# Performance work log

Hardware: AMD Instinct MI355X
Metric: run time of the kernel (lower is better)

## Reference

```python
import jax, jax.numpy as jnp
import numpy as np

NUM_WIRES = 4
NUM_LAYERS = 2


def _apply_ry(state, w, theta):
    # state: (N, 2,2,2,2); theta: scalar or (N,)
    st = jnp.moveaxis(state, 1 + w, -1)
    c = jnp.cos(theta / 2)
    s = jnp.sin(theta / 2)
    # broadcast (N,) -> (N,1,1,1) against st[...,k] of shape (N,2,2,2)
    c = c.reshape(c.shape + (1,) * (st.ndim - 1 - c.ndim))
    s = s.reshape(s.shape + (1,) * (st.ndim - 1 - s.ndim))
    a0, a1 = st[..., 0], st[..., 1]
    st = jnp.stack([c * a0 - s * a1, s * a0 + c * a1], axis=-1)
    return jnp.moveaxis(st, -1, 1 + w)


def _apply_rz(state, w, theta):
    st = jnp.moveaxis(state, 1 + w, -1)
    p = jnp.exp(-0.5j * theta)  # phase on |0>; conj on |1>
    st = jnp.stack([st[..., 0] * p, st[..., 1] * jnp.conj(p)], axis=-1)
    return jnp.moveaxis(st, -1, 1 + w)


def _apply_cnot(state, cw, tw):
    st = jnp.moveaxis(state, (1 + cw, 1 + tw), (-2, -1))
    st = jnp.stack([st[..., 0, :], st[..., 1, ::-1]], axis=-2)
    return jnp.moveaxis(st, (-2, -1), (1 + cw, 1 + tw))


def _circuit(angles, params):
    # angles: (N, 4) RY input angles; params: (L, 4, 3)
    N = angles.shape[0]
    state = jnp.zeros((N, 2, 2, 2, 2), jnp.complex64).at[:, 0, 0, 0, 0].set(1.0)
    for i in range(NUM_WIRES):
        state = _apply_ry(state, i, angles[:, i])
    for l in range(NUM_LAYERS):
        for i in range(NUM_WIRES):
            state = _apply_ry(state, i, params[l, i, 0])
        for i in range(NUM_WIRES - 1):
            state = _apply_cnot(state, i, i + 1)
        for i in range(NUM_WIRES):
            state = _apply_ry(state, i, params[l, i, 1])
        for i in range(NUM_WIRES - 1):
            state = _apply_cnot(state, i + 1, i)
        for i in range(NUM_WIRES):
            state = _apply_rz(state, i, params[l, i, 2])
    probs = state.real ** 2 + state.imag ** 2  # (N,2,2,2,2)
    zs = []
    for i in range(NUM_WIRES):
        axes = tuple(a for a in range(1, 1 + NUM_WIRES) if a != 1 + i)
        marg = probs.sum(axis=axes)  # (N,2)
        zs.append(marg[:, 0] - marg[:, 1])
    return jnp.stack(zs, axis=1)  # (N,4)


def setup_inputs() -> dict:
    key = jax.random.key(0)
    kx, kp = jax.random.split(key)
    x = jax.random.normal(kx, (512, 28, 28), dtype=jnp.float32)
    params = jax.random.normal(kp, (NUM_LAYERS, NUM_WIRES, 3), dtype=jnp.float32)
    return {"x": x, "params": params}


def reference(x, params):
    B = x.shape[0]
    # extract non-overlapping 2x2 patches, row-major over (r, c), patch order
    # [x[r,c], x[r,c+1], x[r+1,c], x[r+1,c+1]] matching .view(batch, -1)
    patches = x.reshape(B, 14, 2, 14, 2).transpose(0, 1, 3, 2, 4).reshape(B, 196, 4)
    # per-patch-location scalar normalization over all batch*4 elements (ddof=1 std)
    n = B * 4
    m = patches.mean(axis=(0, 2), keepdims=True)
    sd = jnp.sqrt(((patches - m) ** 2).sum(axis=(0, 2), keepdims=True) / (n - 1))
    angles = (patches - m) / (sd + 1e-8) * jnp.pi
    z = _circuit(angles.reshape(B * 196, 4), params)  # (B*196, 4)
    return z.reshape(B, 196 * 4).astype(jnp.float32)
```

## Files before the change

kernel.cpp:

```cpp
#include <hip/hip_runtime.h>
#include <math.h>

#define BATCH   512
#define NPATCH  196
#define NSAMP   (BATCH * NPATCH)

__global__ __launch_bounds__(256) void stats_kernel(const float* __restrict__ x,
                                                    float2* __restrict__ stats) {
    const int p = blockIdx.x;
    const int r = p / 14, c = p - r * 14;
    const int t = threadIdx.x;

    float sum = 0.f, sq = 0.f;
    for (int b = t; b < BATCH; b += 256) {
        const float* base = x + b * 784 + (2 * r) * 28 + 2 * c;
        float2 v01 = *(const float2*)base;
        float2 v23 = *(const float2*)(base + 28);
        sum += v01.x + v01.y + v23.x + v23.y;
        sq  += v01.x * v01.x + v01.y * v01.y + v23.x * v23.x + v23.y * v23.y;
    }

    #pragma unroll
    for (int off = 32; off; off >>= 1) {
        sum += __shfl_down(sum, off, 64);
        sq  += __shfl_down(sq,  off, 64);
    }
    __shared__ float ssum[4], ssq[4];
    const int wave = t >> 6, lane = t & 63;
    if (lane == 0) { ssum[wave] = sum; ssq[wave] = sq; }
    __syncthreads();
    if (t == 0) {
        float S = ssum[0] + ssum[1] + ssum[2] + ssum[3];
        float Q = ssq[0]  + ssq[1]  + ssq[2]  + ssq[3];
        const float n = (float)(BATCH * 4);
        float m   = S / n;
        float var = (Q - S * S / n) / (n - 1.0f);
        float sd  = sqrtf(fmaxf(var, 0.f));
        float invh = 0.5f * 3.14159265358979323846f / (sd + 1e-8f);
        stats[p] = make_float2(m, invh);
    }
}

template <int MASK>
__device__ __forceinline__ void ry_gate(float* sr, float* si, float c, float s) {
    #pragma unroll
    for (int i = 0; i < 16; ++i) {
        if ((i & MASK) == 0) {
            const int j = i | MASK;
            float a0 = sr[i], a1 = sr[j];
            sr[i] = c * a0 - s * a1;
            sr[j] = s * a0 + c * a1;
            float b0 = si[i], b1 = si[j];
            si[i] = c * b0 - s * b1;
            si[j] = s * b0 + c * b1;
        }
    }
}

template <int CMASK, int TMASK>
__device__ __forceinline__ void cnot_gate(float* sr, float* si) {
    #pragma unroll
    for (int i = 0; i < 16; ++i) {
        if ((i & CMASK) && !(i & TMASK)) {
            const int j = i | TMASK;
            float t;
            t = sr[i]; sr[i] = sr[j]; sr[j] = t;
            t = si[i]; si[i] = si[j]; si[j] = t;
        }
    }
}

template <int MASK>
__device__ __forceinline__ void rz_gate(float* sr, float* si, float pc, float ps) {
    #pragma unroll
    for (int i = 0; i < 16; ++i) {
        float r = sr[i], im = si[i];
        if (i & MASK) { sr[i] = r * pc - im * ps; si[i] = im * pc + r * ps; }
        else          { sr[i] = r * pc + im * ps; si[i] = im * pc - r * ps; }
    }
}

__global__ __launch_bounds__(256) void circuit_kernel(const float* __restrict__ x,
                                                      const float* __restrict__ params,
                                                      const float2* __restrict__ stats,
                                                      float* __restrict__ out) {
    const int tid = blockIdx.x * 256 + threadIdx.x;
    if (tid >= NSAMP) return;
    const int b = tid / NPATCH;
    const int p = tid - b * NPATCH;
    const int r = p / 14, c = p - r * 14;

    const float* base = x + b * 784 + (2 * r) * 28 + 2 * c;
    float2 v01 = *(const float2*)base;
    float2 v23 = *(const float2*)(base + 28);
    float2 st  = stats[p];

    float h0 = (v01.x - st.x) * st.y;
    float h1 = (v01.y - st.x) * st.y;
    float h2 = (v23.x - st.x) * st.y;
    float h3 = (v23.y - st.x) * st.y;
    float c0, s0, c1, s1, c2, s2, c3, s3;
    __sincosf(h0, &s0, &c0);
    __sincosf(h1, &s1, &c1);
    __sincosf(h2, &s2, &c2);
    __sincosf(h3, &s3, &c3);

    float sr[16], si[16];
    #pragma unroll
    for (int i = 0; i < 16; ++i) {
        sr[i] = ((i & 8) ? s0 : c0) * ((i & 4) ? s1 : c1) *
                ((i & 2) ? s2 : c2) * ((i & 1) ? s3 : c3);
        si[i] = 0.0f;
    }

    float P[24];
    #pragma unroll
    for (int i = 0; i < 24; ++i) P[i] = 0.5f * params[i];

    #pragma unroll
    for (int l = 0; l < 2; ++l) {
        const int o = l * 12;
        float gs, gc;
        __sincosf(P[o + 0], &gs, &gc); ry_gate<8>(sr, si, gc, gs);
        __sincosf(P[o + 3], &gs, &gc); ry_gate<4>(sr, si, gc, gs);
        __sincosf(P[o + 6], &gs, &gc); ry_gate<2>(sr, si, gc, gs);
        __sincosf(P[o + 9], &gs, &gc); ry_gate<1>(sr, si, gc, gs);
        cnot_gate<8, 4>(sr, si);
        cnot_gate<4, 2>(sr, si);
        cnot_gate<2, 1>(sr, si);
        __sincosf(P[o + 1],  &gs, &gc); ry_gate<8>(sr, si, gc, gs);
        __sincosf(P[o + 4],  &gs, &gc); ry_gate<4>(sr, si, gc, gs);
        __sincosf(P[o + 7],  &gs, &gc); ry_gate<2>(sr, si, gc, gs);
        __sincosf(P[o + 10], &gs, &gc); ry_gate<1>(sr, si, gc, gs);
        cnot_gate<4, 8>(sr, si);
        cnot_gate<2, 4>(sr, si);
        cnot_gate<1, 2>(sr, si);
        __sincosf(P[o + 2],  &gs, &gc); rz_gate<8>(sr, si, gc, gs);
        __sincosf(P[o + 5],  &gs, &gc); rz_gate<4>(sr, si, gc, gs);
        __sincosf(P[o + 8],  &gs, &gc); rz_gate<2>(sr, si, gc, gs);
        __sincosf(P[o + 11], &gs, &gc); rz_gate<1>(sr, si, gc, gs);
    }

    float pr[16];
    #pragma unroll
    for (int i = 0; i < 16; ++i) pr[i] = sr[i] * sr[i] + si[i] * si[i];

    float z0 = 0.f, z1 = 0.f, z2 = 0.f, z3 = 0.f;
    #pragma unroll
    for (int i = 0; i < 16; ++i) {
        z0 += (i & 8) ? -pr[i] : pr[i];
        z1 += (i & 4) ? -pr[i] : pr[i];
        z2 += (i & 2) ? -pr[i] : pr[i];
        z3 += (i & 1) ? -pr[i] : pr[i];
    }

    float4 zv = make_float4(z0, z1, z2, z3);
    *(float4*)(out + b * (NPATCH * 4) + p * 4) = zv;
}

extern "C" void kernel_launch(void* const* d_in, const int* in_sizes, int n_in,
                              void* d_out, int out_size, void* d_ws, size_t ws_size,
                              hipStream_t stream) {
    const float* x      = (const float*)d_in[0];
    const float* params = (const float*)d_in[1];
    float*       out    = (float*)d_out;
    float2*      stats  = (float2*)d_ws;

    stats_kernel<<<NPATCH, 256, 0, stream>>>(x, stats);

    const int nblk = (NSAMP + 255) / 256;
    circuit_kernel<<<nblk, 256, 0, stream>>>(x, params, stats, out);
}
```

Before: 65.01 us.

## Fuse stats and circuit kernels into one per-patch block kernel

Merges the per-patch normalization statistics and the quantum circuit simulation into a single kernel, with one block per patch location. Each thread handles two batch samples, reusing the loaded pixels for both the reduction and the circuit. The gate cos/sin values are computed once per block into shared memory rather than by every thread. This removes a kernel launch and the second read of x, but shrinks the grid to 196 blocks, which may underuse the GPU, and the stores to out become strided across the batch.

```diff
diff --git a/kernel.cpp b/kernel.cpp
--- a/kernel.cpp
+++ b/kernel.cpp
@@ -3,43 +3,6 @@
 
 #define BATCH   512
 #define NPATCH  196
-#define NSAMP   (BATCH * NPATCH)
-
-__global__ __launch_bounds__(256) void stats_kernel(const float* __restrict__ x,
-                                                    float2* __restrict__ stats) {
-    const int p = blockIdx.x;
-    const int r = p / 14, c = p - r * 14;
-    const int t = threadIdx.x;
-
-    float sum = 0.f, sq = 0.f;
-    for (int b = t; b < BATCH; b += 256) {
-        const float* base = x + b * 784 + (2 * r) * 28 + 2 * c;
-        float2 v01 = *(const float2*)base;
-        float2 v23 = *(const float2*)(base + 28);
-        sum += v01.x + v01.y + v23.x + v23.y;
-        sq  += v01.x * v01.x + v01.y * v01.y + v23.x * v23.x + v23.y * v23.y;
-    }
-
-    #pragma unroll
-    for (int off = 32; off; off >>= 1) {
-        sum += __shfl_down(sum, off, 64);
-        sq  += __shfl_down(sq,  off, 64);
-    }
-    __shared__ float ssum[4], ssq[4];
-    const int wave = t >> 6, lane = t & 63;
-    if (lane == 0) { ssum[wave] = sum; ssq[wave] = sq; }
-    __syncthreads();
-    if (t == 0) {
-        float S = ssum[0] + ssum[1] + ssum[2] + ssum[3];
-        float Q = ssq[0]  + ssq[1]  + ssq[2]  + ssq[3];
-        const float n = (float)(BATCH * 4);
-        float m   = S / n;
-        float var = (Q - S * S / n) / (n - 1.0f);
-        float sd  = sqrtf(fmaxf(var, 0.f));
-        float invh = 0.5f * 3.14159265358979323846f / (sd + 1e-8f);
-        stats[p] = make_float2(m, invh);
-    }
-}
 
 template <int MASK>
 __device__ __forceinline__ void ry_gate(float* sr, float* si, float c, float s) {
@@ -80,25 +43,8 @@
     }
 }
 
-__global__ __launch_bounds__(256) void circuit_kernel(const float* __restrict__ x,
-                                                      const float* __restrict__ params,
-                                                      const float2* __restrict__ stats,
-                                                      float* __restrict__ out) {
-    const int tid = blockIdx.x * 256 + threadIdx.x;
-    if (tid >= NSAMP) return;
-    const int b = tid / NPATCH;
-    const int p = tid - b * NPATCH;
-    const int r = p / 14, c = p - r * 14;
-
-    const float* base = x + b * 784 + (2 * r) * 28 + 2 * c;
-    float2 v01 = *(const float2*)base;
-    float2 v23 = *(const float2*)(base + 28);
-    float2 st  = stats[p];
-
-    float h0 = (v01.x - st.x) * st.y;
-    float h1 = (v01.y - st.x) * st.y;
-    float h2 = (v23.x - st.x) * st.y;
-    float h3 = (v23.y - st.x) * st.y;
+__device__ __forceinline__ float4 run_circuit(float h0, float h1, float h2, float h3,
+                                              const float* GC, const float* GS) {
     float c0, s0, c1, s1, c2, s2, c3, s3;
     __sincosf(h0, &s0, &c0);
     __sincosf(h1, &s1, &c1);
@@ -113,49 +59,104 @@
         si[i] = 0.0f;
     }
 
-    float P[24];
-    #pragma unroll
-    for (int i = 0; i < 24; ++i) P[i] = 0.5f * params[i];
-
     #pragma unroll
     for (int l = 0; l < 2; ++l) {
         const int o = l * 12;
-        float gs, gc;
-        __sincosf(P[o + 0], &gs, &gc); ry_gate<8>(sr, si, gc, gs);
-        __sincosf(P[o + 3], &gs, &gc); ry_gate<4>(sr, si, gc, gs);
-        __sincosf(P[o + 6], &gs, &gc); ry_gate<2>(sr, si, gc, gs);
-        __sincosf(P[o + 9], &gs, &gc); ry_gate<1>(sr, si, gc, gs);
+        ry_gate<8>(sr, si, GC[o + 0], GS[o + 0]);
+        ry_gate<4>(sr, si, GC[o + 3], GS[o + 3]);
+        ry_gate<2>(sr, si, GC[o + 6], GS[o + 6]);
+        ry_gate<1>(sr, si, GC[o + 9], GS[o + 9]);
         cnot_gate<8, 4>(sr, si);
         cnot_gate<4, 2>(sr, si);
         cnot_gate<2, 1>(sr, si);
-        __sincosf(P[o + 1],  &gs, &gc); ry_gate<8>(sr, si, gc, gs);
-        __sincosf(P[o + 4],  &gs, &gc); ry_gate<4>(sr, si, gc, gs);
-        __sincosf(P[o + 7],  &gs, &gc); ry_gate<2>(sr, si, gc, gs);
-        __sincosf(P[o + 10], &gs, &gc); ry_gate<1>(sr, si, gc, gs);
+        ry_gate<8>(sr, si, GC[o + 1],  GS[o + 1]);
+        ry_gate<4>(sr, si, GC[o + 4],  GS[o + 4]);
+        ry_gate<2>(sr, si, GC[o + 7],  GS[o + 7]);
+        ry_gate<1>(sr, si, GC[o + 10], GS[o + 10]);
         cnot_gate<4, 8>(sr, si);
         cnot_gate<2, 4>(sr, si);
         cnot_gate<1, 2>(sr, si);
-        __sincosf(P[o + 2],  &gs, &gc); rz_gate<8>(sr, si, gc, gs);
-        __sincosf(P[o + 5],  &gs, &gc); rz_gate<4>(sr, si, gc, gs);
-        __sincosf(P[o + 8],  &gs, &gc); rz_gate<2>(sr, si, gc, gs);
-        __sincosf(P[o + 11], &gs, &gc); rz_gate<1>(sr, si, gc, gs);
+        rz_gate<8>(sr, si, GC[o + 2],  GS[o + 2]);
+        rz_gate<4>(sr, si, GC[o + 5],  GS[o + 5]);
+        rz_gate<2>(sr, si, GC[o + 8],  GS[o + 8]);
+        rz_gate<1>(sr, si, GC[o + 11], GS[o + 11]);
     }
-
-    float pr[16];
-    #pragma unroll
-    for (int i = 0; i < 16; ++i) pr[i] = sr[i] * sr[i] + si[i] * si[i];
 
     float z0 = 0.f, z1 = 0.f, z2 = 0.f, z3 = 0.f;
     #pragma unroll
     for (int i = 0; i < 16; ++i) {
-        z0 += (i & 8) ? -pr[i] : pr[i];
-        z1 += (i & 4) ? -pr[i] : pr[i];
-        z2 += (i & 2) ? -pr[i] : pr[i];
-        z3 += (i & 1) ? -pr[i] : pr[i];
+        float pr = sr[i] * sr[i] + si[i] * si[i];
+        z0 += (i & 8) ? -pr : pr;
+        z1 += (i & 4) ? -pr : pr;
+        z2 += (i & 2) ? -pr : pr;
+        z3 += (i & 1) ? -pr : pr;
+    }
+    return make_float4(z0, z1, z2, z3);
+}
+
+__global__ __launch_bounds__(256) void fused_kernel(const float* __restrict__ x,
+                                                    const float* __restrict__ params,
+                                                    float* __restrict__ out) {
+    __shared__ float s_gc[24], s_gs[24];
+    __shared__ float s_sum[4], s_sq[4];
+    __shared__ float s_m, s_invh;
+
+    const int p = blockIdx.x;
+    const int r = p / 14, c = p - r * 14;
+    const int t = threadIdx.x;
+
+    if (t < 24) {
+        float gs, gc;
+        __sincosf(0.5f * params[t], &gs, &gc);
+        s_gc[t] = gc;
+        s_gs[t] = gs;
     }
 
-    float4 zv = make_float4(z0, z1, z2, z3);
-    *(float4*)(out + b * (NPATCH * 4) + p * 4) = zv;
+    const float* base0 = x + t * 784 + (2 * r) * 28 + 2 * c;
+    float2 a01 = *(const float2*)base0;
+    float2 a23 = *(const float2*)(base0 + 28);
+    const float* base1 = base0 + 256 * 784;
+    float2 b01 = *(const float2*)base1;
+    float2 b23 = *(const float2*)(base1 + 28);
+
+    float sum = a01.x + a01.y + a23.x + a23.y + b01.x + b01.y + b23.x + b23.y;
+    float sq  = a01.x * a01.x + a01.y * a01.y + a23.x * a23.x + a23.y * a23.y
+              + b01.x * b01.x + b01.y * b01.y + b23.x * b23.x + b23.y * b23.y;
+
+    #pragma unroll
+    for (int off = 32; off; off >>= 1) {
+        sum += __shfl_down(sum, off, 64);
+        sq  += __shfl_down(sq,  off, 64);
+    }
+    const int wave = t >> 6, lane = t & 63;
+    if (lane == 0) { s_sum[wave] = sum; s_sq[wave] = sq; }
+    __syncthreads();
+    if (t == 0) {
+        float S = s_sum[0] + s_sum[1] + s_sum[2] + s_sum[3];
+        float Q = s_sq[0]  + s_sq[1]  + s_sq[2]  + s_sq[3];
+        const float n = (float)(BATCH * 4);
+        float m   = S / n;
+        float var = (Q - S * S / n) / (n - 1.0f);
+        float sd  = sqrtf(fmaxf(var, 0.f));
+        s_m    = m;
+        s_invh = 0.5f * 3.14159265358979323846f / (sd + 1e-8f);
+    }
+    __syncthreads();
+
+    const float m    = s_m;
+    const float invh = s_invh;
+
+    float GC[24], GS[24];
+    #pragma unroll
+    for (int i = 0; i < 24; ++i) { GC[i] = s_gc[i]; GS[i] = s_gs[i]; }
+
+    float4 z = run_circuit((a01.x - m) * invh, (a01.y - m) * invh,
+                           (a23.x - m) * invh, (a23.y - m) * invh, GC, GS);
+    *(float4*)(out + t * (NPATCH * 4) + p * 4) = z;
+
+    z = run_circuit((b01.x - m) * invh, (b01.y - m) * invh,
+                    (b23.x - m) * invh, (b23.y - m) * invh, GC, GS);
+    *(float4*)(out + (t + 256) * (NPATCH * 4) + p * 4) = z;
 }
 
 extern "C" void kernel_launch(void* const* d_in, const int* in_sizes, int n_in,
@@ -164,10 +165,6 @@
     const float* x      = (const float*)d_in[0];
     const float* params = (const float*)d_in[1];
     float*       out    = (float*)d_out;
-    float2*      stats  = (float2*)d_ws;
 
-    stats_kernel<<<NPATCH, 256, 0, stream>>>(x, stats);
-
-    const int nblk = (NSAMP + 255) / 256;
-    circuit_kernel<<<nblk, 256, 0, stream>>>(x, params, stats, out);
+    fused_kernel<<<NPATCH, 256, 0, stream>>>(x, params, out);
 }
```

Measured after the change: 63.04 us. 1.03x faster.
